# Optimization experiments

Hardware: AMD Instinct MI355X
Metric: run time of the kernel (lower is better)

The kernel has to match this reference:

```python
import jax, jax.numpy as jnp
import numpy as np

B, N, C = 2, 2048, 1024
H = 16
D = C // H  # head_dim = 64

def setup_inputs() -> dict:
    key = jax.random.key(0)
    ks = jax.random.split(key, 5)
    s = 0.02
    return {
        "x": jax.random.normal(ks[0], (B, N, C), dtype=jnp.float32),
        "qkv_w": jax.random.normal(ks[1], (C, 3 * C), dtype=jnp.float32) * s,
        "qkv_b": jax.random.normal(ks[2], (3 * C,), dtype=jnp.float32) * s,
        "proj_w": jax.random.normal(ks[3], (C, C), dtype=jnp.float32) * s,
        "proj_b": jax.random.normal(ks[4], (C,), dtype=jnp.float32) * s,
    }

def reference(x, qkv_w, qkv_b, proj_w, proj_b):
    b, n, c = x.shape
    scale = (c // H) ** -0.5
    qkv = x @ qkv_w + qkv_b                      # (B, N, 3C)
    qkv = qkv.reshape(b, n, 3, H, D)
    q, k, v = jnp.moveaxis(qkv, 2, 0)            # each (B, N, H, D)
    # scores: (B, H, N, N)
    attn = jnp.einsum('bnhd,bmhd->bhnm', q, k) * scale
    attn = jax.nn.softmax(attn, axis=-1)
    out = jnp.einsum('bhnm,bmhd->bnhd', attn, v).reshape(b, n, c)
    out = out @ proj_w + proj_b
    return out
```

## Files before the change

### kernel.cpp

```cpp
#include <hip/hip_runtime.h>
#include <cstdint>
#include <cstddef>

typedef __bf16 bf16x8 __attribute__((ext_vector_type(8)));
typedef float  f32x4  __attribute__((ext_vector_type(4)));
typedef unsigned short u16;
typedef unsigned int u32;

#define MFMA16(a, b, c) __builtin_amdgcn_mfma_f32_16x16x32_bf16((a), (b), (c), 0, 0, 0)
#define ASYNC16(g, l)                                                              \
  __builtin_amdgcn_global_load_lds(                                                \
      (const __attribute__((address_space(1))) unsigned int*)(g),                  \
      (__attribute__((address_space(3))) unsigned int*)(l), 16, 0, 0)

__device__ __forceinline__ u16 f2bf(float f) {
  unsigned u = __builtin_bit_cast(unsigned, f);
  u += 0x7fffu + ((u >> 16) & 1u);
  return (u16)(u >> 16);
}

__device__ __forceinline__ u32 pack_bf2(float a, float b) {
  return (u32)f2bf(a) | ((u32)f2bf(b) << 16);
}

#define SEQ 2048
#define CH  1024
#define NH  16
#define HD  64
#define QSCALE 0.18033688011112042f

__global__ void __launch_bounds__(256) cast_x_kernel(const float* __restrict__ in,
                                                     u16* __restrict__ out) {
  int i = blockIdx.x * 256 + threadIdx.x;
  float4 v = ((const float4*)in)[i];
  ushort4 o;
  o.x = f2bf(v.x); o.y = f2bf(v.y); o.z = f2bf(v.z); o.w = f2bf(v.w);
  ((ushort4*)out)[i] = o;
}

__global__ void __launch_bounds__(256) tcast_kernel(const float* __restrict__ in,
                                                    u16* __restrict__ out, int R, int C) {
  __shared__ u16 t[64][68];
  int c0 = blockIdx.x * 64, r0 = blockIdx.y * 64;
  int tx = threadIdx.x;
  int rr = tx >> 6, cc = tx & 63;
#pragma unroll
  for (int i = 0; i < 16; ++i) {
    int r = i * 4 + rr;
    t[r][cc] = f2bf(in[(size_t)(r0 + r) * C + c0 + cc]);
  }
  __syncthreads();
#pragma unroll
  for (int i = 0; i < 16; ++i) {
    int r = i * 4 + rr;
    out[(size_t)(c0 + r) * R + r0 + cc] = t[cc][r];
  }
}

__global__ void __launch_bounds__(256) tv_kernel(const u16* __restrict__ qkv,
                                                 u16* __restrict__ vt) {
  __shared__ u16 t[64][68];
  int n0 = blockIdx.x * 64;
  int bh = blockIdx.y;
  int b = bh >> 4, h = bh & 15;
  int tx = threadIdx.x;
  int rr = tx >> 6, cc = tx & 63;
  const u16* src = qkv + (size_t)(b * SEQ) * 3072 + 2048 + h * 64;
#pragma unroll
  for (int i = 0; i < 16; ++i) {
    int n = i * 4 + rr;
    t[n][cc] = src[(size_t)(n0 + n) * 3072 + cc];
  }
  __syncthreads();
  u16* dst = vt + (size_t)bh * 64 * SEQ;
#pragma unroll
  for (int i = 0; i < 16; ++i) {
    int d = i * 4 + rr;
    dst[(size_t)d * SEQ + n0 + cc] = t[cc][d];
  }
}

__global__ void __launch_bounds__(256) gemm_kernel(const u16* __restrict__ A,
                                                   const u16* __restrict__ Bt,
                                                   const float* __restrict__ bias,
                                                   u16* __restrict__ outb,
                                                   float* __restrict__ outf,
                                                   int N, int K, int mode) {
  __shared__ alignas(16) u16 As[128 * 32];
  __shared__ alignas(16) u16 Bs[128 * 32];
  int tid = threadIdx.x;
  int lane = tid & 63, wave = tid >> 6;
  int wm = wave >> 1, wn = wave & 1;
  int qr = lane & 15, quad = lane >> 4;
  size_t rowA = (size_t)blockIdx.y * 128;
  size_t rowB = (size_t)blockIdx.x * 128;
  int r0 = tid >> 2, c0 = (tid & 3) << 3;

  const u16* a0 = A + (rowA + r0) * K + c0;
  const u16* b0 = Bt + (rowB + r0) * K + c0;
  size_t step64 = (size_t)64 * K;
  u16* lA = &As[r0 * 32 + c0];
  u16* lB = &Bs[r0 * 32 + c0];

  f32x4 acc[4][4];
#pragma unroll
  for (int mt = 0; mt < 4; ++mt)
#pragma unroll
    for (int nt = 0; nt < 4; ++nt) acc[mt][nt] = (f32x4){0.f, 0.f, 0.f, 0.f};

  for (int k0 = 0; k0 < K; k0 += 32) {
    ASYNC16(a0 + k0, lA);
    ASYNC16(a0 + k0 + step64, lA + 64 * 32);
    ASYNC16(b0 + k0, lB);
    ASYNC16(b0 + k0 + step64, lB + 64 * 32);
    __syncthreads();
    bf16x8 af[4], bfr[4];
#pragma unroll
    for (int mt = 0; mt < 4; ++mt)
      af[mt] = *(const bf16x8*)&As[(wm * 64 + mt * 16 + qr) * 32 + quad * 8];
#pragma unroll
    for (int nt = 0; nt < 4; ++nt)
      bfr[nt] = *(const bf16x8*)&Bs[(wn * 64 + nt * 16 + qr) * 32 + quad * 8];
#pragma unroll
    for (int mt = 0; mt < 4; ++mt)
#pragma unroll
      for (int nt = 0; nt < 4; ++nt)
        acc[mt][nt] = MFMA16(af[mt], bfr[nt], acc[mt][nt]);
    __syncthreads();
  }

#pragma unroll
  for (int nt = 0; nt < 4; ++nt) {
    int col = (int)rowB + wn * 64 + nt * 16 + qr;
    float bv = bias[col];
#pragma unroll
    for (int mt = 0; mt < 4; ++mt) {
      size_t row = rowA + wm * 64 + mt * 16 + quad * 4;
#pragma unroll
      for (int r = 0; r < 4; ++r) {
        float v = acc[mt][nt][r] + bv;
        if (mode == 0) {
          if (col < 1024) v *= QSCALE;
          outb[(row + r) * N + col] = f2bf(v);
        } else {
          outf[(row + r) * N + col] = v;
        }
      }
    }
  }
}

__global__ void __launch_bounds__(256) attn_kernel(const u16* __restrict__ qkv,
                                                   const u16* __restrict__ vt,
                                                   u16* __restrict__ out) {
  __shared__ alignas(16) u16 kbuf[2][64 * 64];
  __shared__ alignas(16) u16 vbuf[2][64 * 64];
  __shared__ alignas(16) u16 pbuf[4][16 * 64];
  int bh = blockIdx.x;
  int b = bh >> 4, h = bh & 15;
  int m0 = blockIdx.y * 64;
  int tid = threadIdx.x;
  int lane = tid & 63, wave = tid >> 6;
  int qr = lane & 15, quad = lane >> 4;

  const u16* kbase = qkv + (size_t)(b * SEQ) * 3072 + 1024 + h * 64;
  const u16* vtbase = vt + (size_t)bh * 64 * SEQ;
  u16* pw = &pbuf[wave][0];

  int srow0 = wave * 16 + (lane >> 3);
  int scs0 = (lane & 7) ^ (srow0 & 7);
  int srow1 = srow0 + 8;
  int scs1 = (lane & 7) ^ (srow1 & 7);

  const u16* qbase = qkv + (size_t)(b * SEQ + m0 + wave * 16) * 3072 + h * 64;
  bf16x8 qf[2];
#pragma unroll
  for (int ks = 0; ks < 2; ++ks)
    qf[ks] = *(const bf16x8*)&qbase[(size_t)qr * 3072 + ks * 32 + quad * 8];

  f32x4 o[4];
  float rsum = 0.f;
#pragma unroll
  for (int dt = 0; dt < 4; ++dt) o[dt] = (f32x4){0.f, 0.f, 0.f, 0.f};

  ASYNC16(kbase + (size_t)srow0 * 3072 + scs0 * 8, &kbuf[0][wave * 1024 + lane * 8]);
  ASYNC16(kbase + (size_t)srow1 * 3072 + scs1 * 8, &kbuf[0][wave * 1024 + 512 + lane * 8]);
  ASYNC16(vtbase + (size_t)srow0 * 2048 + scs0 * 8, &vbuf[0][wave * 1024 + lane * 8]);
  ASYNC16(vtbase + (size_t)srow1 * 2048 + scs1 * 8, &vbuf[0][wave * 1024 + 512 + lane * 8]);

  for (int t = 0; t < 32; ++t) {
    int cur = t & 1;
    __syncthreads();

    if (t + 1 < 32) {
      int nx = (t + 1) * 64;
      int o2 = cur ^ 1;
      ASYNC16(kbase + (size_t)(nx + srow0) * 3072 + scs0 * 8, &kbuf[o2][wave * 1024 + lane * 8]);
      ASYNC16(kbase + (size_t)(nx + srow1) * 3072 + scs1 * 8, &kbuf[o2][wave * 1024 + 512 + lane * 8]);
      ASYNC16(vtbase + (size_t)srow0 * 2048 + nx + scs0 * 8, &vbuf[o2][wave * 1024 + lane * 8]);
      ASYNC16(vtbase + (size_t)srow1 * 2048 + nx + scs1 * 8, &vbuf[o2][wave * 1024 + 512 + lane * 8]);
    }

    const u16* kb = &kbuf[cur][0];
    const u16* vb = &vbuf[cur][0];

    bf16x8 kf[4][2];
#pragma unroll
    for (int nt = 0; nt < 4; ++nt)
#pragma unroll
      for (int ks = 0; ks < 2; ++ks)
        kf[nt][ks] = *(const bf16x8*)&kb[(nt * 16 + qr) * 64 + (((ks * 4 + quad) ^ (qr & 7)) << 3)];

#pragma unroll
    for (int nt = 0; nt < 4; ++nt) {
      f32x4 z = (f32x4){0.f, 0.f, 0.f, 0.f};
      z = MFMA16(kf[nt][0], qf[0], z);
      z = MFMA16(kf[nt][1], qf[1], z);
      float p0 = __builtin_amdgcn_exp2f(z[0]);
      float p1 = __builtin_amdgcn_exp2f(z[1]);
      float p2 = __builtin_amdgcn_exp2f(z[2]);
      float p3 = __builtin_amdgcn_exp2f(z[3]);
      rsum += (p0 + p1) + (p2 + p3);
      uint2 pk;
      pk.x = pack_bf2(p0, p1);
      pk.y = pack_bf2(p2, p3);
      int nb = nt * 16 + quad * 4;
      int addr = qr * 64 + ((((nb >> 3) ^ (qr & 7)) << 3) | (nb & 7));
      *(uint2*)&pw[addr] = pk;
    }

    bf16x8 vf[4][2];
#pragma unroll
    for (int dt = 0; dt < 4; ++dt)
#pragma unroll
      for (int ks = 0; ks < 2; ++ks)
        vf[dt][ks] = *(const bf16x8*)&vb[(dt * 16 + qr) * 64 + (((ks * 4 + quad) ^ (qr & 7)) << 3)];

    bf16x8 pf[2];
#pragma unroll
    for (int ks = 0; ks < 2; ++ks)
      pf[ks] = *(const bf16x8*)&pw[qr * 64 + (((ks * 4 + quad) ^ (qr & 7)) << 3)];

#pragma unroll
    for (int dt = 0; dt < 4; ++dt) {
      o[dt] = MFMA16(pf[0], vf[dt][0], o[dt]);
      o[dt] = MFMA16(pf[1], vf[dt][1], o[dt]);
    }
  }

  rsum += __shfl_xor(rsum, 16, 64);
  rsum += __shfl_xor(rsum, 32, 64);

  u16* obase = out + (size_t)(b * SEQ + m0 + wave * 16) * CH + h * 64;
#pragma unroll
  for (int r = 0; r < 4; ++r) {
    float l = __shfl(rsum, quad * 4 + r, 64);
    float inv = 1.0f / l;
#pragma unroll
    for (int dt = 0; dt < 4; ++dt)
      obase[(size_t)(quad * 4 + r) * CH + dt * 16 + qr] = f2bf(o[dt][r] * inv);
  }
}

extern "C" void kernel_launch(void* const* d_in, const int* in_sizes, int n_in,
                              void* d_out, int out_size, void* d_ws, size_t ws_size,
                              hipStream_t stream) {
  const float* x      = (const float*)d_in[0];
  const float* qkv_w  = (const float*)d_in[1];
  const float* qkv_b  = (const float*)d_in[2];
  const float* proj_w = (const float*)d_in[3];
  const float* proj_b = (const float*)d_in[4];
  float* out = (float*)d_out;

  char* w = (char*)d_ws;
  u16* qkv_bf = (u16*)w;
  u16* xb     = (u16*)(w + 25165824);
  u16* wprojt = (u16*)(w + 25165824 + 8388608);
  u16* wqkvt  = (u16*)(w + 25165824 + 8388608 + 2097152);
  u16* attn_bf = xb;
  u16* vt      = wqkvt;

  cast_x_kernel<<<4096, 256, 0, stream>>>(x, xb);
  tcast_kernel<<<dim3(48, 16), 256, 0, stream>>>(qkv_w, wqkvt, 1024, 3072);
  tcast_kernel<<<dim3(16, 16), 256, 0, stream>>>(proj_w, wprojt, 1024, 1024);
  gemm_kernel<<<dim3(24, 32), 256, 0, stream>>>(xb, wqkvt, qkv_b, qkv_bf, nullptr, 3072, 1024, 0);
  tv_kernel<<<dim3(32, 32), 256, 0, stream>>>(qkv_bf, vt);
  attn_kernel<<<dim3(32, 32), 256, 0, stream>>>(qkv_bf, vt, attn_bf);
  gemm_kernel<<<dim3(8, 32), 256, 0, stream>>>(attn_bf, wprojt, proj_b, nullptr, out, 1024, 1024, 1);
}
```

Measured before the change: 219.5 us.

## Double attention query tile per wave, MFMA row sums, smaller proj GEMM tiles

The attention kernel now processes 32 query rows per wave (128 per block), so each K/V tile loaded into shared memory is reused across twice as many queries, and the block count halves. Row sums of the softmax numerators come from an extra MFMA against a ones vector instead of scalar adds and cross-lane shuffles, and bf16 packing uses the native conversion. The projection GEMM is templated to use 64-row A tiles, doubling its grid to fill more compute units. In exchange the attention kernel holds more registers and shared memory per block, which may lower occupancy.

```diff
diff --git a/kernel.cpp b/kernel.cpp
--- a/kernel.cpp
+++ b/kernel.cpp
@@ -3,8 +3,10 @@
 #include <cstddef>
 
 typedef __bf16 bf16x8 __attribute__((ext_vector_type(8)));
+typedef __bf16 bf16x2v __attribute__((ext_vector_type(2)));
+typedef unsigned short u16;
+typedef u16 u16x8v __attribute__((ext_vector_type(8)));
 typedef float  f32x4  __attribute__((ext_vector_type(4)));
-typedef unsigned short u16;
 typedef unsigned int u32;
 
 #define MFMA16(a, b, c) __builtin_amdgcn_mfma_f32_16x16x32_bf16((a), (b), (c), 0, 0, 0)
@@ -19,8 +21,11 @@
   return (u16)(u >> 16);
 }
 
-__device__ __forceinline__ u32 pack_bf2(float a, float b) {
-  return (u32)f2bf(a) | ((u32)f2bf(b) << 16);
+__device__ __forceinline__ u32 cvt2(float a, float b) {
+  bf16x2v t;
+  t[0] = (__bf16)a;
+  t[1] = (__bf16)b;
+  return __builtin_bit_cast(u32, t);
 }
 
 #define SEQ 2048
@@ -80,19 +85,21 @@
   }
 }
 
+template <int MT>
 __global__ void __launch_bounds__(256) gemm_kernel(const u16* __restrict__ A,
                                                    const u16* __restrict__ Bt,
                                                    const float* __restrict__ bias,
                                                    u16* __restrict__ outb,
                                                    float* __restrict__ outf,
                                                    int N, int K, int mode) {
-  __shared__ alignas(16) u16 As[128 * 32];
+  constexpr int R = MT * 32;
+  __shared__ alignas(16) u16 As[R * 32];
   __shared__ alignas(16) u16 Bs[128 * 32];
   int tid = threadIdx.x;
   int lane = tid & 63, wave = tid >> 6;
   int wm = wave >> 1, wn = wave & 1;
   int qr = lane & 15, quad = lane >> 4;
-  size_t rowA = (size_t)blockIdx.y * 128;
+  size_t rowA = (size_t)blockIdx.y * R;
   size_t rowB = (size_t)blockIdx.x * 128;
   int r0 = tid >> 2, c0 = (tid & 3) << 3;
 
@@ -102,27 +109,28 @@
   u16* lA = &As[r0 * 32 + c0];
   u16* lB = &Bs[r0 * 32 + c0];
 
-  f32x4 acc[4][4];
-#pragma unroll
-  for (int mt = 0; mt < 4; ++mt)
+  f32x4 acc[MT][4];
+#pragma unroll
+  for (int mt = 0; mt < MT; ++mt)
 #pragma unroll
     for (int nt = 0; nt < 4; ++nt) acc[mt][nt] = (f32x4){0.f, 0.f, 0.f, 0.f};
 
   for (int k0 = 0; k0 < K; k0 += 32) {
-    ASYNC16(a0 + k0, lA);
-    ASYNC16(a0 + k0 + step64, lA + 64 * 32);
+#pragma unroll
+    for (int i = 0; i < R / 64; ++i)
+      ASYNC16(a0 + k0 + i * step64, lA + i * 64 * 32);
     ASYNC16(b0 + k0, lB);
     ASYNC16(b0 + k0 + step64, lB + 64 * 32);
     __syncthreads();
-    bf16x8 af[4], bfr[4];
-#pragma unroll
-    for (int mt = 0; mt < 4; ++mt)
-      af[mt] = *(const bf16x8*)&As[(wm * 64 + mt * 16 + qr) * 32 + quad * 8];
+    bf16x8 af[MT], bfr[4];
+#pragma unroll
+    for (int mt = 0; mt < MT; ++mt)
+      af[mt] = *(const bf16x8*)&As[(wm * (MT * 16) + mt * 16 + qr) * 32 + quad * 8];
 #pragma unroll
     for (int nt = 0; nt < 4; ++nt)
       bfr[nt] = *(const bf16x8*)&Bs[(wn * 64 + nt * 16 + qr) * 32 + quad * 8];
 #pragma unroll
-    for (int mt = 0; mt < 4; ++mt)
+    for (int mt = 0; mt < MT; ++mt)
 #pragma unroll
       for (int nt = 0; nt < 4; ++nt)
         acc[mt][nt] = MFMA16(af[mt], bfr[nt], acc[mt][nt]);
@@ -134,8 +142,8 @@
     int col = (int)rowB + wn * 64 + nt * 16 + qr;
     float bv = bias[col];
 #pragma unroll
-    for (int mt = 0; mt < 4; ++mt) {
-      size_t row = rowA + wm * 64 + mt * 16 + quad * 4;
+    for (int mt = 0; mt < MT; ++mt) {
+      size_t row = rowA + wm * (MT * 16) + mt * 16 + quad * 4;
 #pragma unroll
       for (int r = 0; r < 4; ++r) {
         float v = acc[mt][nt][r] + bv;
@@ -155,10 +163,10 @@
                                                    u16* __restrict__ out) {
   __shared__ alignas(16) u16 kbuf[2][64 * 64];
   __shared__ alignas(16) u16 vbuf[2][64 * 64];
-  __shared__ alignas(16) u16 pbuf[4][16 * 64];
+  __shared__ alignas(16) u16 pbuf[4][32 * 64];
   int bh = blockIdx.x;
   int b = bh >> 4, h = bh & 15;
-  int m0 = blockIdx.y * 64;
+  int m0 = blockIdx.y * 128;
   int tid = threadIdx.x;
   int lane = tid & 63, wave = tid >> 6;
   int qr = lane & 15, quad = lane >> 4;
@@ -172,16 +180,23 @@
   int srow1 = srow0 + 8;
   int scs1 = (lane & 7) ^ (srow1 & 7);
 
-  const u16* qbase = qkv + (size_t)(b * SEQ + m0 + wave * 16) * 3072 + h * 64;
-  bf16x8 qf[2];
-#pragma unroll
-  for (int ks = 0; ks < 2; ++ks)
-    qf[ks] = *(const bf16x8*)&qbase[(size_t)qr * 3072 + ks * 32 + quad * 8];
-
-  f32x4 o[4];
-  float rsum = 0.f;
-#pragma unroll
-  for (int dt = 0; dt < 4; ++dt) o[dt] = (f32x4){0.f, 0.f, 0.f, 0.f};
+  const u16* qbase = qkv + (size_t)(b * SEQ + m0 + wave * 32) * 3072 + h * 64;
+  bf16x8 qf[2][2];
+#pragma unroll
+  for (int mt = 0; mt < 2; ++mt)
+#pragma unroll
+    for (int ks = 0; ks < 2; ++ks)
+      qf[mt][ks] = *(const bf16x8*)&qbase[(size_t)(mt * 16 + qr) * 3072 + ks * 32 + quad * 8];
+
+  const bf16x8 vone = __builtin_bit_cast(bf16x8, (u16x8v)((u16)0x3F80));
+
+  f32x4 o[2][4], l5[2];
+#pragma unroll
+  for (int mt = 0; mt < 2; ++mt) {
+    l5[mt] = (f32x4){0.f, 0.f, 0.f, 0.f};
+#pragma unroll
+    for (int dt = 0; dt < 4; ++dt) o[mt][dt] = (f32x4){0.f, 0.f, 0.f, 0.f};
+  }
 
   ASYNC16(kbase + (size_t)srow0 * 3072 + scs0 * 8, &kbuf[0][wave * 1024 + lane * 8]);
   ASYNC16(kbase + (size_t)srow1 * 3072 + scs1 * 8, &kbuf[0][wave * 1024 + 512 + lane * 8]);
@@ -212,22 +227,23 @@
         kf[nt][ks] = *(const bf16x8*)&kb[(nt * 16 + qr) * 64 + (((ks * 4 + quad) ^ (qr & 7)) << 3)];
 
 #pragma unroll
-    for (int nt = 0; nt < 4; ++nt) {
-      f32x4 z = (f32x4){0.f, 0.f, 0.f, 0.f};
-      z = MFMA16(kf[nt][0], qf[0], z);
-      z = MFMA16(kf[nt][1], qf[1], z);
-      float p0 = __builtin_amdgcn_exp2f(z[0]);
-      float p1 = __builtin_amdgcn_exp2f(z[1]);
-      float p2 = __builtin_amdgcn_exp2f(z[2]);
-      float p3 = __builtin_amdgcn_exp2f(z[3]);
-      rsum += (p0 + p1) + (p2 + p3);
-      uint2 pk;
-      pk.x = pack_bf2(p0, p1);
-      pk.y = pack_bf2(p2, p3);
-      int nb = nt * 16 + quad * 4;
-      int addr = qr * 64 + ((((nb >> 3) ^ (qr & 7)) << 3) | (nb & 7));
-      *(uint2*)&pw[addr] = pk;
-    }
+    for (int mt = 0; mt < 2; ++mt)
+#pragma unroll
+      for (int nt = 0; nt < 4; ++nt) {
+        f32x4 z = (f32x4){0.f, 0.f, 0.f, 0.f};
+        z = MFMA16(kf[nt][0], qf[mt][0], z);
+        z = MFMA16(kf[nt][1], qf[mt][1], z);
+        float p0 = __builtin_amdgcn_exp2f(z[0]);
+        float p1 = __builtin_amdgcn_exp2f(z[1]);
+        float p2 = __builtin_amdgcn_exp2f(z[2]);
+        float p3 = __builtin_amdgcn_exp2f(z[3]);
+        uint2 pk;
+        pk.x = cvt2(p0, p1);
+        pk.y = cvt2(p2, p3);
+        int nb = nt * 16 + quad * 4;
+        int addr = (mt * 16 + qr) * 64 + ((((nb >> 3) ^ (qr & 7)) << 3) | (nb & 7));
+        *(uint2*)&pw[addr] = pk;
+      }
 
     bf16x8 vf[4][2];
 #pragma unroll
@@ -236,30 +252,36 @@
       for (int ks = 0; ks < 2; ++ks)
         vf[dt][ks] = *(const bf16x8*)&vb[(dt * 16 + qr) * 64 + (((ks * 4 + quad) ^ (qr & 7)) << 3)];
 
-    bf16x8 pf[2];
-#pragma unroll
-    for (int ks = 0; ks < 2; ++ks)
-      pf[ks] = *(const bf16x8*)&pw[qr * 64 + (((ks * 4 + quad) ^ (qr & 7)) << 3)];
-
-#pragma unroll
-    for (int dt = 0; dt < 4; ++dt) {
-      o[dt] = MFMA16(pf[0], vf[dt][0], o[dt]);
-      o[dt] = MFMA16(pf[1], vf[dt][1], o[dt]);
+    bf16x8 pf[2][2];
+#pragma unroll
+    for (int mt = 0; mt < 2; ++mt)
+#pragma unroll
+      for (int ks = 0; ks < 2; ++ks)
+        pf[mt][ks] =
+            *(const bf16x8*)&pw[(mt * 16 + qr) * 64 + (((ks * 4 + quad) ^ (qr & 7)) << 3)];
+
+#pragma unroll
+    for (int mt = 0; mt < 2; ++mt) {
+#pragma unroll
+      for (int dt = 0; dt < 4; ++dt) {
+        o[mt][dt] = MFMA16(pf[mt][0], vf[dt][0], o[mt][dt]);
+        o[mt][dt] = MFMA16(pf[mt][1], vf[dt][1], o[mt][dt]);
+      }
+      l5[mt] = MFMA16(pf[mt][0], vone, l5[mt]);
+      l5[mt] = MFMA16(pf[mt][1], vone, l5[mt]);
     }
   }
 
-  rsum += __shfl_xor(rsum, 16, 64);
-  rsum += __shfl_xor(rsum, 32, 64);
-
-  u16* obase = out + (size_t)(b * SEQ + m0 + wave * 16) * CH + h * 64;
-#pragma unroll
-  for (int r = 0; r < 4; ++r) {
-    float l = __shfl(rsum, quad * 4 + r, 64);
-    float inv = 1.0f / l;
-#pragma unroll
-    for (int dt = 0; dt < 4; ++dt)
-      obase[(size_t)(quad * 4 + r) * CH + dt * 16 + qr] = f2bf(o[dt][r] * inv);
-  }
+  u16* obase = out + (size_t)(b * SEQ + m0 + wave * 32) * CH + h * 64;
+#pragma unroll
+  for (int mt = 0; mt < 2; ++mt)
+#pragma unroll
+    for (int r = 0; r < 4; ++r) {
+      float inv = 1.0f / l5[mt][r];
+#pragma unroll
+      for (int dt = 0; dt < 4; ++dt)
+        obase[(size_t)(mt * 16 + quad * 4 + r) * CH + dt * 16 + qr] = f2bf(o[mt][dt][r] * inv);
+    }
 }
 
 extern "C" void kernel_launch(void* const* d_in, const int* in_sizes, int n_in,
@@ -283,8 +305,8 @@
   cast_x_kernel<<<4096, 256, 0, stream>>>(x, xb);
   tcast_kernel<<<dim3(48, 16), 256, 0, stream>>>(qkv_w, wqkvt, 1024, 3072);
   tcast_kernel<<<dim3(16, 16), 256, 0, stream>>>(proj_w, wprojt, 1024, 1024);
-  gemm_kernel<<<dim3(24, 32), 256, 0, stream>>>(xb, wqkvt, qkv_b, qkv_bf, nullptr, 3072, 1024, 0);
+  gemm_kernel<4><<<dim3(24, 32), 256, 0, stream>>>(xb, wqkvt, qkv_b, qkv_bf, nullptr, 3072, 1024, 0);
   tv_kernel<<<dim3(32, 32), 256, 0, stream>>>(qkv_bf, vt);
-  attn_kernel<<<dim3(32, 32), 256, 0, stream>>>(qkv_bf, vt, attn_bf);
-  gemm_kernel<<<dim3(8, 32), 256, 0, stream>>>(attn_bf, wprojt, proj_b, nullptr, out, 1024, 1024, 1);
-}
+  attn_kernel<<<dim3(32, 16), 256, 0, stream>>>(qkv_bf, vt, attn_bf);
+  gemm_kernel<2><<<dim3(8, 64), 256, 0, stream>>>(attn_bf, wprojt, proj_b, nullptr, out, 1024, 1024, 1);
+}
```

Result: faster. 213.1 us (-2.9%).
